# Optimization experiments

Measured on AMD Instinct MI355X. Metric: run time of the kernel, lower is better.

## Reference

```python
import jax, jax.numpy as jnp
import numpy as np

B, N, E_PER = 32, 2048, 16384
DIN, H = 128, 128
RATIO = 0.3


def setup_inputs() -> dict:
    key = jax.random.key(0)
    ks = jax.random.split(key, 16)
    s_in = 1.0 / np.sqrt(DIN)
    s_h = 1.0 / np.sqrt(H)
    inp = {
        "x": jax.random.normal(ks[0], (B * N, DIN), dtype=jnp.float32),
        "edge_src": jax.random.randint(ks[1], (B, E_PER), 0, N, dtype=jnp.int32),
        "edge_dst": jax.random.randint(ks[2], (B, E_PER), 0, N, dtype=jnp.int32),
        # SAGEConv layer 1: lin_l (neighbor agg, with bias), lin_r (root, no bias)
        "Wl1": jax.random.normal(ks[3], (H, DIN), dtype=jnp.float32) * s_in,
        "bl1": jnp.zeros((H,), dtype=jnp.float32),
        "Wr1": jax.random.normal(ks[4], (H, DIN), dtype=jnp.float32) * s_in,
        # SAGEConv layer 2
        "Wl2": jax.random.normal(ks[5], (H, H), dtype=jnp.float32) * s_h,
        "bl2": jnp.zeros((H,), dtype=jnp.float32),
        "Wr2": jax.random.normal(ks[6], (H, H), dtype=jnp.float32) * s_h,
        # TopKPooling score weight
        "pool_w": jax.random.normal(ks[7], (H,), dtype=jnp.float32) * s_h,
        # classifier MLP
        "Wc1": jax.random.normal(ks[8], (H, H), dtype=jnp.float32) * s_h,
        "bc1": jnp.zeros((H,), dtype=jnp.float32),
        "Wc2": jax.random.normal(ks[9], (1, H), dtype=jnp.float32) * s_h,
        "bc2": jnp.zeros((1,), dtype=jnp.float32),
    }
    return inp


def _sage_conv(x, src, dst, n_total, Wl, bl, Wr):
    # mean-aggregate neighbor messages: msg flows src -> dst
    msg = x[src]                                                   # [E, D] gather
    agg = jax.ops.segment_sum(msg, dst, num_segments=n_total)      # [Nt, D]
    deg = jax.ops.segment_sum(jnp.ones_like(dst, dtype=x.dtype), dst,
                              num_segments=n_total)
    agg = agg / jnp.maximum(deg, 1.0)[:, None]
    return agg @ Wl.T + bl + x @ Wr.T


def _forward(x, edge_src, edge_dst, Wl1, bl1, Wr1, Wl2, bl2, Wr2,
             pool_w, Wc1, bc1, Wc2, bc2):
    n_total = x.shape[0]
    # offset per-graph node ids into the disjoint-union batch
    off = (jnp.arange(B, dtype=edge_src.dtype) * N)[:, None]
    src = (edge_src + off).reshape(-1)
    dst = (edge_dst + off).reshape(-1)

    x = jax.nn.relu(_sage_conv(x, src, dst, n_total, Wl1, bl1, Wr1))
    x = jax.nn.relu(_sage_conv(x, src, dst, n_total, Wl2, bl2, Wr2))

    # TopKPooling: score = tanh(x . w / ||w||); keep top ceil(ratio*N) per graph
    score = jnp.tanh(x @ pool_w / jnp.linalg.norm(pool_w))         # [Nt]
    k = int(np.ceil(RATIO * N))                                    # 615
    vals, idx = jax.lax.top_k(score.reshape(B, N), k)              # [B, k]
    xg = x.reshape(B, N, -1)
    x_sel = jnp.take_along_axis(xg, idx[..., None], axis=1)        # [B, k, H]
    x_sel = x_sel * vals[..., None]                                # gate by score

    # global mean pool over kept nodes, then MLP classifier
    emb = x_sel.mean(axis=1)                                       # [B, H]
    h = jax.nn.relu(emb @ Wc1.T + bc1)
    return (h @ Wc2.T + bc2).squeeze(-1)                           # [B]


def reference(x, edge_src, edge_dst, Wl1, bl1, Wr1, Wl2, bl2, Wr2,
              pool_w, Wc1, bc1, Wc2, bc2):
    return _forward(x, edge_src, edge_dst, Wl1, bl1, Wr1, Wl2, bl2, Wr2,
                    pool_w, Wc1, bc1, Wc2, bc2)
```

## Files before the change

### kernel.cpp

```cpp
#include <hip/hip_runtime.h>
#include <stdint.h>
#include <math.h>

#define NB    32
#define NNODE 2048
#define NT    (NB*NNODE)
#define EPB   16384
#define ETOT  (NB*EPB)
#define DF    128
#define KSEL  615
#define EMAX  512

typedef __attribute__((ext_vector_type(8))) short bf16x8;
typedef __attribute__((ext_vector_type(4))) float f32x4;

__device__ __forceinline__ unsigned short f2bf(float f){
  uint32_t u = __float_as_uint(f);
  u += 0x7FFFu + ((u>>16)&1u);
  return (unsigned short)(u>>16);
}
__device__ __forceinline__ void split2(float f, unsigned short& hi, unsigned short& lo){
  unsigned short h = f2bf(f);
  float fh = __uint_as_float(((uint32_t)h)<<16);
  hi = h;
  lo = f2bf(f - fh);
}
__device__ __forceinline__ uint32_t f2mono(float f){
  uint32_t u = __float_as_uint(f);
  return (u & 0x80000000u) ? ~u : (u | 0x80000000u);
}
__device__ __forceinline__ float mono2f(uint32_t m){
  uint32_t u = (m & 0x80000000u) ? (m ^ 0x80000000u) : ~m;
  return __uint_as_float(u);
}
__device__ __forceinline__ f32x4 ntload4(const float* p){
  return __builtin_nontemporal_load((const f32x4*)p);
}
__device__ __forceinline__ void ntstore(float v, float* p){
  __builtin_nontemporal_store(v, p);
}

__global__ void k_deg(const int* __restrict__ edst, uint32_t* __restrict__ deg,
                      const float* __restrict__ Wl1, const float* __restrict__ Wr1,
                      const float* __restrict__ Wl2, const float* __restrict__ Wr2,
                      unsigned short* __restrict__ Bpk){
  const int bid = blockIdx.x;
  if (bid < ETOT/256){
    int e = bid*256 + threadIdx.x;
    int g = e >> 14;
    atomicAdd(&deg[g*NNODE + edst[e]], 1u);
  } else {
    int tt = (bid - ETOT/256)*256 + threadIdx.x;
    int layer = tt >> 12;
    int t2 = tt & 4095;
    const float* Wl = layer ? Wl2 : Wl1;
    const float* Wr = layer ? Wr2 : Wr1;
    unsigned short* B = Bpk + (size_t)layer*65536;
    int lane = t2 & 63;
    int ct   = (t2>>6) & 7;
    int ks   = (t2>>9) & 7;
    int c  = ct*16 + (lane & 15);
    int k0 = ks*32 + ((lane>>4)<<3);
    size_t base = ((size_t)((ks*8+ct)*2)*64 + lane)*8;
    #pragma unroll
    for (int j=0;j<8;++j){
      int k = k0 + j;
      float v = (k < DF) ? Wl[c*DF + k] : Wr[c*DF + (k-DF)];
      unsigned short h, l; split2(v, h, l);
      B[base + j]       = h;
      B[base + 512 + j] = l;
    }
  }
}

__global__ __launch_bounds__(1024) void k_scan1(const uint32_t* __restrict__ deg,
                        uint32_t* __restrict__ rowptr, uint32_t* __restrict__ bsum){
  __shared__ uint32_t sh[1024];
  int t = threadIdx.x; int base = blockIdx.x*1024;
  uint32_t v = deg[base+t];
  sh[t] = v;
  for (int off=1; off<1024; off<<=1){
    __syncthreads();
    uint32_t a = (t>=off) ? sh[t-off] : 0u;
    __syncthreads();
    sh[t] += a;
  }
  rowptr[base+t] = sh[t] - v;
  if (t==1023) bsum[blockIdx.x] = sh[1023];
}

__global__ void k_scan2(uint32_t* __restrict__ bsum){
  __shared__ uint32_t sh[64];
  int t = threadIdx.x;
  uint32_t v = bsum[t]; sh[t] = v;
  for (int off=1; off<64; off<<=1){
    __syncthreads();
    uint32_t a = (t>=off) ? sh[t-off] : 0u;
    __syncthreads();
    sh[t] += a;
  }
  bsum[t] = sh[t] - v;
}

__global__ __launch_bounds__(1024) void k_scan3(uint32_t* __restrict__ rowptr,
                                                const uint32_t* __restrict__ bsum){
  int i = blockIdx.x*1024 + threadIdx.x;
  rowptr[i] += bsum[i>>10];
  if (i==0) rowptr[NT] = ETOT;
}

__global__ void k_scatter(const int* __restrict__ esrc, const int* __restrict__ edst,
                          const uint32_t* __restrict__ rowptr, uint32_t* __restrict__ deg,
                          int* __restrict__ col){
  int e = blockIdx.x*256 + threadIdx.x;
  int g = e >> 14;
  int d = g*NNODE + edst[e];
  int s = g*NNODE + esrc[e];
  uint32_t old = atomicSub(&deg[d], 1u);
  col[rowptr[d] + old - 1u] = s;
}

template<int LAYER>
__global__ __launch_bounds__(128, 4) void k_sage(
    const float* __restrict__ Xin, const uint32_t* __restrict__ rowptr,
    const int* __restrict__ col, const unsigned short* __restrict__ Bpk,
    const float* __restrict__ bias, float* __restrict__ OUT,
    const float* __restrict__ pw, float* __restrict__ scores)
{
  __shared__ float smemA[32][132];
  __shared__ int lcol[EMAX];
  __shared__ uint32_t lrp[33];

  const int t = threadIdx.x;
  const int g = blockIdx.x & 31, jb = blockIdx.x >> 5;
  const int rowBase = g*NNODE + jb*32;

  if (t < 33) lrp[t] = rowptr[rowBase + t];
  const uint32_t e0 = rowptr[rowBase];
  const int ecnt = (int)(rowptr[rowBase + 32] - e0);
  for (int i=t; i<ecnt && i<EMAX; i+=128) lcol[i] = col[e0+i];

  const int l = t & 63, wid = t >> 6;
  const int q = l >> 4, c16 = l & 15;
  const int arow = rowBase + wid*16 + c16;
  f32x4 own[8];
  #pragma unroll
  for (int ks4=0; ks4<4; ++ks4){
    const float* s = Xin + (size_t)arow*DF + ks4*32 + q*8;
    own[ks4*2]   = ntload4(s);
    own[ks4*2+1] = ntload4(s+4);
  }
  __syncthreads();

  {
    const int grp = t >> 5, c = t & 31;
    auto gather = [&](auto colAt){
      for (int n=grp; n<32; n+=4){
        uint32_t b = lrp[n] - e0, e = lrp[n+1] - e0;
        f32x4 a = {0.f,0.f,0.f,0.f};
        uint32_t k = b;
        for (; k+8<=e; k+=8){
          int s0=colAt(k),  s1=colAt(k+1), s2=colAt(k+2), s3=colAt(k+3),
              s4=colAt(k+4),s5=colAt(k+5), s6=colAt(k+6), s7=colAt(k+7);
          f32x4 v0=ntload4(Xin+(size_t)s0*DF+4*c), v1=ntload4(Xin+(size_t)s1*DF+4*c),
                v2=ntload4(Xin+(size_t)s2*DF+4*c), v3=ntload4(Xin+(size_t)s3*DF+4*c),
                v4=ntload4(Xin+(size_t)s4*DF+4*c), v5=ntload4(Xin+(size_t)s5*DF+4*c),
                v6=ntload4(Xin+(size_t)s6*DF+4*c), v7=ntload4(Xin+(size_t)s7*DF+4*c);
          a += ((v0+v1)+(v2+v3)) + ((v4+v5)+(v6+v7));
        }
        for (; k+4<=e; k+=4){
          int s0=colAt(k), s1=colAt(k+1), s2=colAt(k+2), s3=colAt(k+3);
          f32x4 v0=ntload4(Xin+(size_t)s0*DF+4*c), v1=ntload4(Xin+(size_t)s1*DF+4*c),
                v2=ntload4(Xin+(size_t)s2*DF+4*c), v3=ntload4(Xin+(size_t)s3*DF+4*c);
          a += (v0+v1)+(v2+v3);
        }
        for (; k<e; ++k){
          a += ntload4(Xin+(size_t)colAt(k)*DF+4*c);
        }
        float invd = 1.0f / (float)((e>b)?(e-b):1u);
        *(f32x4*)&smemA[n][4*c] = a * invd;
      }
    };
    if (ecnt <= EMAX) gather([&](uint32_t k){ return lcol[k]; });
    else              gather([&](uint32_t k){ return col[e0+k]; });
  }
  __syncthreads();

  f32x4 acc[8];
  #pragma unroll
  for (int ct=0; ct<8; ++ct) acc[ct] = (f32x4){0.f,0.f,0.f,0.f};

  #pragma unroll
  for (int ks=0; ks<8; ++ks){
    f32x4 A0, A1;
    if (ks < 4){
      const float* s = &smemA[wid*16 + c16][ks*32 + q*8];
      A0 = *(const f32x4*)s; A1 = *(const f32x4*)(s+4);
    } else {
      A0 = own[(ks-4)*2]; A1 = own[(ks-4)*2+1];
    }
    float v[8] = {A0.x,A0.y,A0.z,A0.w,A1.x,A1.y,A1.z,A1.w};
    bf16x8 ahi, alo;
    #pragma unroll
    for (int j=0;j<8;++j){
      unsigned short h, lo_; split2(v[j], h, lo_);
      ahi[j] = (short)h; alo[j] = (short)lo_;
    }
    const unsigned short* bp = Bpk + (size_t)ks*8192 + l*8;
    #pragma unroll
    for (int ct=0; ct<8; ++ct){
      bf16x8 bhi = *(const bf16x8*)(bp + ct*1024);
      bf16x8 blo = *(const bf16x8*)(bp + ct*1024 + 512);
      acc[ct] = __builtin_amdgcn_mfma_f32_16x16x32_bf16(ahi, bhi, acc[ct], 0,0,0);
      acc[ct] = __builtin_amdgcn_mfma_f32_16x16x32_bf16(ahi, blo, acc[ct], 0,0,0);
      acc[ct] = __builtin_amdgcn_mfma_f32_16x16x32_bf16(alo, bhi, acc[ct], 0,0,0);
    }
  }

  const int rowOut = rowBase + wid*16;
  if constexpr (LAYER==1){
    #pragma unroll
    for (int ct=0; ct<8; ++ct){
      int c = ct*16 + c16;
      float bv = bias[c];
      #pragma unroll
      for (int r=0; r<4; ++r){
        int grow = rowOut + q*4 + r;
        ntstore(fmaxf(acc[ct][r] + bv, 0.f), &OUT[(size_t)grow*DF + c]);
      }
    }
  } else {
    float ov[8][4];
    float pwv[8];
    float n2 = 0.f;
    #pragma unroll
    for (int ct=0; ct<8; ++ct){ pwv[ct] = pw[ct*16 + c16]; n2 += pwv[ct]*pwv[ct]; }
    n2 += __shfl_xor(n2,8,16); n2 += __shfl_xor(n2,4,16);
    n2 += __shfl_xor(n2,2,16); n2 += __shfl_xor(n2,1,16);
    float nrm = sqrtf(n2);
    #pragma unroll
    for (int ct=0; ct<8; ++ct){
      int c = ct*16 + c16;
      float bv = bias[c];
      #pragma unroll
      for (int r=0; r<4; ++r){
        int grow = rowOut + q*4 + r;
        float o = fmaxf(acc[ct][r] + bv, 0.f);
        ntstore(o, &OUT[(size_t)grow*DF + c]);
        ov[ct][r] = o;
      }
    }
    #pragma unroll
    for (int r=0; r<4; ++r){
      float p = 0.f;
      #pragma unroll
      for (int ct=0; ct<8; ++ct) p += ov[ct][r]*pwv[ct];
      p += __shfl_xor(p,8,16); p += __shfl_xor(p,4,16);
      p += __shfl_xor(p,2,16); p += __shfl_xor(p,1,16);
      if (c16 == 0) scores[rowOut + q*4 + r] = tanhf(p/nrm);
    }
  }
}

__global__ __launch_bounds__(1024) void k_topk(
    const float* __restrict__ scores, const float* __restrict__ H,
    const float* __restrict__ Wc1, const float* __restrict__ bc1,
    const float* __restrict__ Wc2, const float* __restrict__ bc2,
    float* __restrict__ out)
{
  __shared__ uint32_t keys[NNODE];
  __shared__ uint32_t hist[64];
  __shared__ uint32_t wsum[16];
  __shared__ uint32_t sh_b, sh_rank, sh_cnt;
  __shared__ unsigned short selidx[KSEL+1];
  __shared__ float selval[KSEL+1];
  __shared__ float part[8*DF];
  __shared__ float emb[DF];
  __shared__ float hred[DF];

  const int t = threadIdx.x; const int b = blockIdx.x;
  const int lane = t & 63, wid = t >> 6;
  const float* sc = scores + b*NNODE;

  for (int i=t; i<NNODE; i+=1024) keys[i] = f2mono(sc[i]);
  __syncthreads();

  uint32_t prefix = 0, prefmask = 0, rank = KSEL, cntT = 0;
  #pragma unroll
  for (int lev=0; lev<6; ++lev){
    const int shift = (lev<5) ? (26 - 6*lev) : 0;
    const uint32_t bmask = (lev<5) ? 63u : 3u;
    if (t < 64) hist[t] = 0;
    __syncthreads();
    for (int i=t; i<NNODE; i+=1024){
      uint32_t k = keys[i];
      if ((k & prefmask) == prefix) atomicAdd(&hist[(k>>shift)&bmask], 1u);
    }
    __syncthreads();
    if (t < 64){
      uint32_t x = hist[t];
      #pragma unroll
      for (int off=1; off<64; off<<=1){
        uint32_t y = __shfl_down(x, off, 64);
        if (t + off < 64) x += y;
      }
      uint32_t above = __shfl_down(x, 1, 64);
      if (t == 63) above = 0;
      if (above < rank && rank <= x){
        sh_b = (uint32_t)t; sh_rank = rank - above; sh_cnt = x - above;
      }
    }
    __syncthreads();
    prefix |= (sh_b << shift);
    prefmask |= (bmask << shift);
    rank = sh_rank; cntT = sh_cnt;
    __syncthreads();
  }
  const uint32_t T = prefix;
  const uint32_t m = rank;

  uint32_t k0 = keys[2*t], k1 = keys[2*t+1];
  uint32_t eq0 = (k0 == T), eq1 = (k1 == T);
  uint32_t eqr0 = 0, eqr1 = 0;

  if (m != cntT){
    uint32_t v = eq0 + eq1, x = v;
    #pragma unroll
    for (int off=1; off<64; off<<=1){
      uint32_t y = __shfl_up(x, off, 64);
      if (lane >= off) x += y;
    }
    if (lane == 63) wsum[wid] = x;
    __syncthreads();
    if (wid == 0){
      uint32_t s = (lane < 16) ? wsum[lane] : 0;
      #pragma unroll
      for (int off=1; off<16; off<<=1){
        uint32_t y = __shfl_up(s, off, 64);
        if (lane >= off) s += y;
      }
      if (lane < 16) wsum[lane] = s;
    }
    __syncthreads();
    uint32_t excl = (wid ? wsum[wid-1] : 0) + x - v;
    eqr0 = excl; eqr1 = excl + eq0;
    __syncthreads();
  }

  uint32_t sel0 = (k0 > T) || (eq0 && eqr0 < m);
  uint32_t sel1 = (k1 > T) || (eq1 && eqr1 < m);
  {
    uint32_t v = sel0 + sel1, x = v;
    #pragma unroll
    for (int off=1; off<64; off<<=1){
      uint32_t y = __shfl_up(x, off, 64);
      if (lane >= off) x += y;
    }
    if (lane == 63) wsum[wid] = x;
    __syncthreads();
    if (wid == 0){
      uint32_t s = (lane < 16) ? wsum[lane] : 0;
      #pragma unroll
      for (int off=1; off<16; off<<=1){
        uint32_t y = __shfl_up(s, off, 64);
        if (lane >= off) s += y;
      }
      if (lane < 16) wsum[lane] = s;
    }
    __syncthreads();
    uint32_t excl = (wid ? wsum[wid-1] : 0) + x - v;
    if (sel0){ selidx[excl] = (unsigned short)(2*t);   selval[excl] = mono2f(k0); }
    if (sel1){ selidx[excl+sel0] = (unsigned short)(2*t+1); selval[excl+sel0] = mono2f(k1); }
  }
  __syncthreads();

  const int pg = t >> 7, f = t & (DF-1);
  const float* Hb = H + (size_t)b*NNODE*DF;
  float accv = 0.f;
  int s2 = pg;
  for (; s2+24 < KSEL; s2 += 32){
    int i0=selidx[s2], i1=selidx[s2+8], i2=selidx[s2+16], i3=selidx[s2+24];
    float w0=selval[s2], w1=selval[s2+8], w2=selval[s2+16], w3=selval[s2+24];
    float v0=Hb[(size_t)i0*DF+f], v1=Hb[(size_t)i1*DF+f],
          v2=Hb[(size_t)i2*DF+f], v3=Hb[(size_t)i3*DF+f];
    accv += w0*v0 + w1*v1 + w2*v2 + w3*v3;
  }
  for (; s2<KSEL; s2+=8) accv += selval[s2]*Hb[(size_t)selidx[s2]*DF+f];
  part[pg*DF + f] = accv;
  __syncthreads();
  if (t < DF){
    float e = 0.f;
    for (int g2=0; g2<8; ++g2) e += part[g2*DF + t];
    emb[t] = e / (float)KSEL;
  }
  __syncthreads();
  if (t < DF){
    float hv = bc1[t];
    const float* wr = Wc1 + t*DF;
    for (int f2=0; f2<DF; ++f2) hv = fmaf(emb[f2], wr[f2], hv);
    hred[t] = fmaxf(hv, 0.f) * Wc2[t];
  }
  __syncthreads();
  if (t == 0){
    float o = bc2[0];
    for (int c2=0; c2<DF; ++c2) o += hred[c2];
    out[b] = o;
  }
}

extern "C" void kernel_launch(void* const* d_in, const int* in_sizes, int n_in,
                              void* d_out, int out_size, void* d_ws, size_t ws_size,
                              hipStream_t stream)
{
  (void)in_sizes; (void)n_in; (void)out_size; (void)ws_size;
  const float* x   = (const float*)d_in[0];
  const int* esrc  = (const int*)d_in[1];
  const int* edst  = (const int*)d_in[2];
  const float* Wl1 = (const float*)d_in[3];
  const float* bl1 = (const float*)d_in[4];
  const float* Wr1 = (const float*)d_in[5];
  const float* Wl2 = (const float*)d_in[6];
  const float* bl2 = (const float*)d_in[7];
  const float* Wr2 = (const float*)d_in[8];
  const float* pw  = (const float*)d_in[9];
  const float* Wc1 = (const float*)d_in[10];
  const float* bc1 = (const float*)d_in[11];
  const float* Wc2 = (const float*)d_in[12];
  const float* bc2 = (const float*)d_in[13];
  float* out = (float*)d_out;

  char* ws = (char*)d_ws;
  float*    H1     = (float*)   (ws + 0);
  float*    H2     = (float*)   (ws + 33554432);
  uint32_t* deg    = (uint32_t*)(ws + 67108864);
  uint32_t* rowptr = (uint32_t*)(ws + 67371008);
  int*      col    = (int*)     (ws + 67633408);
  float*    scores = (float*)   (ws + 69730560);
  uint32_t* bsum   = (uint32_t*)(ws + 69992704);
  unsigned short* Bpk = (unsigned short*)(ws + 69992960);

  hipMemsetAsync(deg, 0, NT*sizeof(uint32_t), stream);

  k_deg    <<<ETOT/256 + 32, 256, 0, stream>>>(edst, deg, Wl1, Wr1, Wl2, Wr2, Bpk);
  k_scan1  <<<64, 1024, 0, stream>>>(deg, rowptr, bsum);
  k_scan2  <<<1, 64, 0, stream>>>(bsum);
  k_scan3  <<<64, 1024, 0, stream>>>(rowptr, bsum);
  k_scatter<<<ETOT/256, 256, 0, stream>>>(esrc, edst, rowptr, deg, col);

  k_sage<1><<<NT/32, 128, 0, stream>>>(x,  rowptr, col, Bpk,         bl1,
                                       H1, nullptr, nullptr);
  k_sage<2><<<NT/32, 128, 0, stream>>>(H1, rowptr, col, Bpk + 65536, bl2,
                                       H2, pw, scores);

  k_topk<<<NB, 1024, 0, stream>>>(scores, H2, Wc1, bc1, Wc2, bc2, out);
}
```

Baseline: 184.4 us.

## Software-pipeline neighbor gather across a contiguous edge range per thread group

The gather stage now gives each thread group a contiguous block of 8 rows and walks their combined edge range in a flat loop. It prefetches the next 8 neighbor rows into registers while accumulating the current 8 and flushes each row's mean when a row boundary is crossed. This replaces per-row loops with separate remainder tails and keeps more loads in flight across short rows. The own-row loads now happen after the gather. Nontemporal loads and stores are replaced with ordinary cached accesses, so gathered and output data can stay in cache, at the cost of extra registers for the double buffer.

```diff
diff --git a/kernel.cpp b/kernel.cpp
--- a/kernel.cpp
+++ b/kernel.cpp
@@ -32,12 +32,6 @@
 __device__ __forceinline__ float mono2f(uint32_t m){
   uint32_t u = (m & 0x80000000u) ? (m ^ 0x80000000u) : ~m;
   return __uint_as_float(u);
-}
-__device__ __forceinline__ f32x4 ntload4(const float* p){
-  return __builtin_nontemporal_load((const f32x4*)p);
-}
-__device__ __forceinline__ void ntstore(float v, float* p){
-  __builtin_nontemporal_store(v, p);
 }
 
 __global__ void k_deg(const int* __restrict__ edst, uint32_t* __restrict__ deg,
@@ -129,62 +123,79 @@
 {
   __shared__ float smemA[32][132];
   __shared__ int lcol[EMAX];
-  __shared__ uint32_t lrp[33];
+  __shared__ uint32_t lrpl[33];
 
   const int t = threadIdx.x;
   const int g = blockIdx.x & 31, jb = blockIdx.x >> 5;
   const int rowBase = g*NNODE + jb*32;
 
-  if (t < 33) lrp[t] = rowptr[rowBase + t];
   const uint32_t e0 = rowptr[rowBase];
+  if (t < 33) lrpl[t] = rowptr[rowBase + t] - e0;
   const int ecnt = (int)(rowptr[rowBase + 32] - e0);
   for (int i=t; i<ecnt && i<EMAX; i+=128) lcol[i] = col[e0+i];
+  __syncthreads();
+
+  {
+    const int grp = t >> 5, c = t & 31;
+    int cur = grp*8;
+    const int curEnd = grp*8 + 8;
+    f32x4 accv = {0.f,0.f,0.f,0.f};
+
+    auto flushrow = [&](){
+      uint32_t d = lrpl[cur+1] - lrpl[cur];
+      float invd = 1.0f / (float)(d ? d : 1u);
+      *(f32x4*)&smemA[cur][4*c] = accv * invd;
+      accv = (f32x4){0.f,0.f,0.f,0.f};
+      cur++;
+    };
+
+    const uint32_t kb = lrpl[grp*8], ke = lrpl[curEnd];
+    auto run = [&](auto colAt){
+      f32x4 v[8], w[8];
+      #pragma unroll
+      for (int j=0;j<8;++j){
+        uint32_t kk = kb + j;
+        int s = colAt(kk < ke ? kk : kb);
+        v[j] = *(const f32x4*)(Xin + (size_t)s*DF + 4*c);
+      }
+      for (uint32_t k = kb; k < ke; k += 8){
+        #pragma unroll
+        for (int j=0;j<8;++j){
+          uint32_t kk = k + 8 + j;
+          int s = colAt(kk < ke ? kk : k);
+          w[j] = *(const f32x4*)(Xin + (size_t)s*DF + 4*c);
+        }
+        #pragma unroll
+        for (int j=0;j<8;++j){
+          uint32_t kk = k + j;
+          if (kk < ke){
+            while (lrpl[cur+1] <= kk) flushrow();
+            accv += v[j];
+          }
+        }
+        #pragma unroll
+        for (int j=0;j<8;++j) v[j] = w[j];
+      }
+    };
+    if (kb < ke){
+      if (ecnt <= EMAX) run([&](uint32_t k){ return lcol[k]; });
+      else              run([&](uint32_t k){ return col[e0+k]; });
+    }
+    while (cur < curEnd) flushrow();
+  }
+  __syncthreads();
 
   const int l = t & 63, wid = t >> 6;
   const int q = l >> 4, c16 = l & 15;
   const int arow = rowBase + wid*16 + c16;
+
   f32x4 own[8];
   #pragma unroll
   for (int ks4=0; ks4<4; ++ks4){
     const float* s = Xin + (size_t)arow*DF + ks4*32 + q*8;
-    own[ks4*2]   = ntload4(s);
-    own[ks4*2+1] = ntload4(s+4);
-  }
-  __syncthreads();
-
-  {
-    const int grp = t >> 5, c = t & 31;
-    auto gather = [&](auto colAt){
-      for (int n=grp; n<32; n+=4){
-        uint32_t b = lrp[n] - e0, e = lrp[n+1] - e0;
-        f32x4 a = {0.f,0.f,0.f,0.f};
-        uint32_t k = b;
-        for (; k+8<=e; k+=8){
-          int s0=colAt(k),  s1=colAt(k+1), s2=colAt(k+2), s3=colAt(k+3),
-              s4=colAt(k+4),s5=colAt(k+5), s6=colAt(k+6), s7=colAt(k+7);
-          f32x4 v0=ntload4(Xin+(size_t)s0*DF+4*c), v1=ntload4(Xin+(size_t)s1*DF+4*c),
-                v2=ntload4(Xin+(size_t)s2*DF+4*c), v3=ntload4(Xin+(size_t)s3*DF+4*c),
-                v4=ntload4(Xin+(size_t)s4*DF+4*c), v5=ntload4(Xin+(size_t)s5*DF+4*c),
-                v6=ntload4(Xin+(size_t)s6*DF+4*c), v7=ntload4(Xin+(size_t)s7*DF+4*c);
-          a += ((v0+v1)+(v2+v3)) + ((v4+v5)+(v6+v7));
-        }
-        for (; k+4<=e; k+=4){
-          int s0=colAt(k), s1=colAt(k+1), s2=colAt(k+2), s3=colAt(k+3);
-          f32x4 v0=ntload4(Xin+(size_t)s0*DF+4*c), v1=ntload4(Xin+(size_t)s1*DF+4*c),
-                v2=ntload4(Xin+(size_t)s2*DF+4*c), v3=ntload4(Xin+(size_t)s3*DF+4*c);
-          a += (v0+v1)+(v2+v3);
-        }
-        for (; k<e; ++k){
-          a += ntload4(Xin+(size_t)colAt(k)*DF+4*c);
-        }
-        float invd = 1.0f / (float)((e>b)?(e-b):1u);
-        *(f32x4*)&smemA[n][4*c] = a * invd;
-      }
-    };
-    if (ecnt <= EMAX) gather([&](uint32_t k){ return lcol[k]; });
-    else              gather([&](uint32_t k){ return col[e0+k]; });
-  }
-  __syncthreads();
+    own[ks4*2]   = *(const f32x4*)s;
+    own[ks4*2+1] = *(const f32x4*)(s+4);
+  }
 
   f32x4 acc[8];
   #pragma unroll
@@ -226,7 +237,7 @@
       #pragma unroll
       for (int r=0; r<4; ++r){
         int grow = rowOut + q*4 + r;
-        ntstore(fmaxf(acc[ct][r] + bv, 0.f), &OUT[(size_t)grow*DF + c]);
+        OUT[(size_t)grow*DF + c] = fmaxf(acc[ct][r] + bv, 0.f);
       }
     }
   } else {
@@ -246,7 +257,7 @@
       for (int r=0; r<4; ++r){
         int grow = rowOut + q*4 + r;
         float o = fmaxf(acc[ct][r] + bv, 0.f);
-        ntstore(o, &OUT[(size_t)grow*DF + c]);
+        OUT[(size_t)grow*DF + c] = o;
         ov[ct][r] = o;
       }
     }
```

New measurement: 159.0 us. 1.16x faster.
